# Kernel tuning notes

Hardware: AMD Instinct MI355X
Metric: run time of the kernel (lower is better)

Reference implementation:

```python
import jax, jax.numpy as jnp
import numpy as np

SAMPLE_RATE = 22050
N_FILTER_BANKS = 64
HOP_LENGTH = 512
BATCH = 4
N_FRAMES = 500
N_SAMPLES = N_FRAMES * HOP_LENGTH


def _frame_mean_weights(n_frames, n_samples):
    """Per-frame weights w s.t. mean over time of linear(align_corners=True)
    upsampling of a length-n_frames signal equals w @ signal (exact same math,
    since the interpolation is linear in the frame values)."""
    pos = jnp.linspace(0.0, n_frames - 1.0, n_samples)
    lo = jnp.clip(jnp.floor(pos).astype(jnp.int32), 0, n_frames - 2)
    frac = pos - lo
    w = jnp.zeros(n_frames, dtype=jnp.float32)
    w = w.at[lo].add(1.0 - frac).at[lo + 1].add(frac)
    return w / n_samples


def setup_inputs() -> dict:
    key = jax.random.key(0)
    k1, k2 = jax.random.split(key)
    filter_magnitudes = jax.random.uniform(k1, (BATCH, N_FRAMES, N_FILTER_BANKS), dtype=jnp.float32)
    noise = jax.random.normal(k2, (BATCH, N_SAMPLES), dtype=jnp.float32)
    return {"filter_magnitudes": filter_magnitudes, "noise": noise}


def reference(filter_magnitudes, noise):
    B, n_frames, n_banks = filter_magnitudes.shape
    n_samples = noise.shape[1]

    noise_fft = jnp.fft.rfft(noise, axis=1)                      # (B, n_freq) complex
    freqs = jnp.fft.rfftfreq(n_samples, 1.0 / SAMPLE_RATE)       # (n_freq,)
    filter_freqs = jnp.logspace(np.log10(20.0), np.log10(SAMPLE_RATE / 2.0), n_banks).astype(jnp.float32)

    # mean over time of the linearly-upsampled magnitudes (exact, no big buffer)
    mean_w = _frame_mean_weights(n_frames, n_samples)            # (n_frames,)
    mean_mag = jnp.einsum('bfk,f->bk', filter_magnitudes, mean_w)  # (B, n_banks)

    # vectorized log-distance filterbank weights: (n_freq, n_banks)
    D = jnp.log(freqs + 1e-7)[:, None] - jnp.log(filter_freqs + 1e-7)[None, :]
    W = jnp.exp(-(D ** 2) / 0.5)
    W = W / (W.sum(axis=1, keepdims=True) + 1e-7)

    filter_response = mean_mag @ W.T                              # (B, n_freq)
    filtered_fft = noise_fft * filter_response
    return jnp.fft.irfft(filtered_fft, n=n_samples, axis=1)      # (B, n_samples)
```

## Files before the change

kernel.cpp:

```cpp
#include <hip/hip_runtime.h>
#include <math.h>

#define NS 256000
#define N1 512
#define N2 500
#define PI_F 3.14159265358979323846f

typedef float2 cplx;

__device__ __forceinline__ cplx cadd(cplx a, cplx b){ return make_float2(a.x+b.x, a.y+b.y); }
__device__ __forceinline__ cplx csub(cplx a, cplx b){ return make_float2(a.x-b.x, a.y-b.y); }
__device__ __forceinline__ cplx cmul(cplx a, cplx b){ return make_float2(a.x*b.x-a.y*b.y, a.x*b.y+a.y*b.x); }
__device__ __forceinline__ cplx cmulc(cplx a, cplx b){ return make_float2(a.x*b.x+a.y*b.y, a.y*b.x-a.x*b.y); }
__device__ __forceinline__ cplx crotf(cplx v, float ang){
    float sn = __sinf(ang), cs = __cosf(ang);
    return make_float2(v.x*cs - v.y*sn, v.x*sn + v.y*cs);
}
__device__ __forceinline__ int PX(int e){ return e + (e>>4); }
__device__ __forceinline__ int rev8_3(int k){ return ((k&7)<<6) | (k&0x38) | (k>>6); }

#define U1PAD 545
#define U2PAD 537
#define WFENCE() asm volatile("s_waitcnt lgkmcnt(0)" ::: "memory")
#define LDS_BARRIER() do{ asm volatile("s_waitcnt lgkmcnt(0)" ::: "memory"); __builtin_amdgcn_s_barrier(); }while(0)

template<bool INV>
__device__ __forceinline__ void dft4(const cplx* a, cplx* b){
    cplx t0=cadd(a[0],a[2]), t1=csub(a[0],a[2]), t2=cadd(a[1],a[3]), t3=csub(a[1],a[3]);
    b[0]=cadd(t0,t2); b[2]=csub(t0,t2);
    if(!INV){ b[1]=make_float2(t1.x+t3.y, t1.y-t3.x); b[3]=make_float2(t1.x-t3.y, t1.y+t3.x); }
    else    { b[1]=make_float2(t1.x-t3.y, t1.y+t3.x); b[3]=make_float2(t1.x+t3.y, t1.y-t3.x); }
}

template<bool INV>
__device__ __forceinline__ void dft8(const cplx* a, cplx* b){
    cplx ev[4]={a[0],a[2],a[4],a[6]}, od[4]={a[1],a[3],a[5],a[7]};
    cplx C[4], D[4];
    dft4<INV>(ev, C); dft4<INV>(od, D);
    const float s = 0.70710678118654752f;
    const float sg = INV ? 1.f : -1.f;
    cplx d1 = cmul(D[1], make_float2( s, sg*s));
    cplx d2 = cmul(D[2], make_float2(0.f, sg ));
    cplx d3 = cmul(D[3], make_float2(-s, sg*s));
    b[0]=cadd(C[0],D[0]); b[4]=csub(C[0],D[0]);
    b[1]=cadd(C[1],d1);   b[5]=csub(C[1],d1);
    b[2]=cadd(C[2],d2);   b[6]=csub(C[2],d2);
    b[3]=cadd(C[3],d3);   b[7]=csub(C[3],d3);
}

template<bool INV>
__device__ __forceinline__ void dft5(const cplx* a, cplx* b){
    const float c1=0.30901699437494742f, s1=0.95105651629515357f;
    const float c2=-0.80901699437494745f, s2=0.58778525229247312f;
    const float sg = INV ? 1.f : -1.f;
    cplx W[5];
    W[0]=make_float2(1.f,0.f);
    W[1]=make_float2(c1, sg*s1); W[2]=make_float2(c2, sg*s2);
    W[3]=make_float2(c2,-sg*s2); W[4]=make_float2(c1,-sg*s1);
#pragma unroll
    for(int u=0;u<5;++u){
        cplx acc = a[0];
        int idx = 0;
#pragma unroll
        for(int r=1;r<5;++r){
            idx += u; if(idx >= 5) idx -= 5;
            acc = cadd(acc, cmul(a[r], W[idx]));
        }
        b[u] = acc;
    }
}

template<int R, int L, int TMUL, bool INV, int NN>
__device__ __forceinline__ void wstage(cplx* Uw, const cplx* tab, int lane){
    constexpr int m = L / R;
    constexpr int nb = NN / R;
    constexpr int NIT = (nb + 63) / 64;
    cplx a[NIT][R];
    cplx wt[NIT][R];
    int  bs[NIT];
#pragma unroll
    for(int it=0; it<NIT; ++it){
        int beta = lane + it*64;
        int blk = beta / m;
        int j = beta - blk*m;
        bs[it] = blk*L + j;
        if(beta < nb){
#pragma unroll
            for(int t=0;t<R;++t) a[it][t] = Uw[PX(bs[it] + m*t)];
#pragma unroll
            for(int t=1;t<R;++t) wt[it][t] = tab[TMUL*j*t];
        }
    }
#pragma unroll
    for(int it=0; it<NIT; ++it){
        int beta = lane + it*64;
        if(beta < nb){
            if(INV){
#pragma unroll
                for(int t=1;t<R;++t) a[it][t] = cmulc(a[it][t], wt[it][t]);
            }
            cplx bb[R];
            if constexpr (R==4) dft4<INV>(a[it], bb);
            else if constexpr (R==5) dft5<INV>(a[it], bb);
            else dft8<INV>(a[it], bb);
            if(!INV){
#pragma unroll
                for(int t=1;t<R;++t) bb[t] = cmul(bb[t], wt[it][t]);
            }
#pragma unroll
            for(int t=0;t<R;++t) Uw[PX(bs[it] + m*t)] = bb[t];
        }
    }
}

template<int R, int L, int TMUL, bool INV>
__device__ __forceinline__ void wstage2(cplx* Uc, const cplx* tab, int lane, int h){
    constexpr int m = L / R;
    constexpr int nb = 500 / R;
    constexpr int HB = (nb + 1) / 2;
    const int lim = h ? (nb - HB) : HB;
    if(lane < lim){
        int beta = h*HB + lane;
        int blk = beta / m;
        int j = beta - blk*m;
        int base = blk*L + j;
        cplx a[R];
#pragma unroll
        for(int t=0;t<R;++t) a[t] = Uc[PX(base + m*t)];
        cplx wt[R];
#pragma unroll
        for(int t=1;t<R;++t) wt[t] = tab[TMUL*j*t];
        if(INV){
#pragma unroll
            for(int t=1;t<R;++t) a[t] = cmulc(a[t], wt[t]);
        }
        cplx bb[R];
        if constexpr (R==4) dft4<INV>(a,bb);
        else if constexpr (R==5) dft5<INV>(a,bb);
        else dft8<INV>(a,bb);
        if(!INV){
#pragma unroll
            for(int t=1;t<R;++t) bb[t] = cmul(bb[t], wt[t]);
        }
#pragma unroll
        for(int t=0;t<R;++t) Uc[PX(base + m*t)] = bb[t];
    }
}

template<int NTAB, int NTHR>
__device__ __forceinline__ void build_tab(cplx* tab, int tid){
    const float step = -2.f*PI_F/(float)NTAB;
    for(int i = tid; i < NTAB; i += NTHR){
        float a = step*(float)i;
        tab[i] = make_float2(__cosf(a), __sinf(a));
    }
}

__device__ __forceinline__ int p2k2(int p){
    int t1 = p/100; int r = p - 100*t1;
    int t2 = r/20;  r -= 20*t2;
    int t3 = r>>2;  int t4 = r & 3;
    return t1 + 5*t2 + 25*t3 + 125*t4;
}
__device__ __forceinline__ int k22p(int k){
    int t1 = k % 5; int k5 = k/5;
    int t2 = k5 % 5; int k25 = k5/5;
    int t3 = k25 % 5; int t4 = k25/5;
    return 100*t1 + 20*t2 + 4*t3 + t4;
}
__device__ __forceinline__ int colord(int q){
    int j = q>>1, w = q&1;
    if(j == 0) return w ? 256 : 0;
    return w ? 512 - j : j;
}
__device__ __forceinline__ int xcd_chunk(int bid, int n){
    int q = n>>3, r = n&7;
    int x = bid&7, idx = bid>>3;
    return (x < r ? x*(q+1) : r*(q+1) + (x-r)*q) + idx;
}

__device__ __forceinline__ void hpair(cplx Z1, cplx Z2, float ha, float hb,
                                      cplx* zk, cplx* znk){
    float xr = 0.5f*(Z1.x + Z2.x), xi = 0.5f*(Z1.y - Z2.y);
    float yr = 0.5f*(Z1.y + Z2.y), yi = -0.5f*(Z1.x - Z2.x);
    *zk  = make_float2(ha*xr - hb*yi, ha*xi + hb*yr);
    *znk = make_float2(ha*xr + hb*yi, hb*yr - ha*xi);
}

__global__ void __launch_bounds__(256) kFused1(const float* __restrict__ fm,
                                               const float* __restrict__ noise,
                                               float* __restrict__ mmL,
                                               cplx* __restrict__ Y){
    __shared__ float Aarr[500];
    __shared__ float wfr[500];
    __shared__ float part[256];
    __shared__ cplx tab[512];
    __shared__ cplx U[4][U1PAD];
    const int bid = blockIdx.x, tid = threadIdx.x;
    if(bid < 4){
        const int b = bid;
        for(int f = tid; f < 500; f += 256){
            long long i0 = ((long long)f*255999LL + 498LL)/499LL;
            long long i1 = ((long long)(f+1)*255999LL + 498LL)/499LL;
            long long cnt = i1 - i0;
            long long sumi = (i0 + i1 - 1)*cnt/2;
            long long num = 499LL*sumi - cnt*(long long)f*255999LL;
            Aarr[f] = (float)((double)num / 255999.0);
        }
        __syncthreads();
        for(int f = tid; f < 500; f += 256){
            long long i0 = ((long long)f*255999LL + 498LL)/499LL;
            long long i1 = ((long long)(f+1)*255999LL + 498LL)/499LL;
            double w;
            if(f < 499) w = (double)(i1 - i0) - (double)Aarr[f] + (f > 0 ? (double)Aarr[f-1] : 0.0);
            else        w = (double)Aarr[498] + 1.0;
            wfr[f] = (float)(w / (double)NS);
        }
        __syncthreads();
        const int k = tid & 63, seg = tid >> 6;
        float acc = 0.f;
        for(int f = seg*125; f < seg*125 + 125; ++f)
            acc += wfr[f] * fm[(b*500 + f)*64 + k];
        part[seg*64 + k] = acc;
        __syncthreads();
        if(tid < 64) mmL[b*64 + tid] = part[tid] + part[64+tid] + part[128+tid] + part[192+tid];
        return;
    }
    if(bid == 4){
        if(tid < 64){
            double a = log10(20.0), b2 = log10(11025.0);
            double e = a + (b2 - a)*(double)tid/63.0;
            float ff = (float)pow(10.0, e);
            mmL[256 + tid] = logf(ff + 1e-7f);
        }
        return;
    }
    const int g = xcd_chunk(bid - 5, 250);
    const int s = g / 125;
    const int n2base = (g - s*125) * 4;
    const int lane = tid & 63, w = tid >> 6;
    build_tab<512,256>(tab, tid);
    const float* xa = noise + (size_t)(2*s)*NS + n2base;
    const float* xb = noise + (size_t)(2*s+1)*NS + n2base;
#pragma unroll
    for(int k=0;k<8;++k){
        int i = tid + 256*k;
        int n1 = i >> 2, ws = i & 3;
        U[ws][PX(n1)] = make_float2(xa[n1*500 + ws], xb[n1*500 + ws]);
    }
    __syncthreads();
    cplx* Uw = U[w];
    wstage<8,512, 1,false,512>(Uw, tab, lane); WFENCE();
    wstage<8, 64, 8,false,512>(Uw, tab, lane); WFENCE();
    wstage<8,  8,64,false,512>(Uw, tab, lane); WFENCE();
    const int n2 = n2base + w;
    cplx* yp = Y + ((size_t)s*500 + n2)*512;
    const float tw = -2.f*PI_F/(float)NS;
#pragma unroll
    for(int t=0;t<8;++t){
        int q = lane + 64*t;
        int c = colord(q);
        cplx v = Uw[PX(rev8_3(c))];
        v = crotf(v, tw*(float)(n2*c));
        yp[q] = v;
    }
}

__global__ void __launch_bounds__(256) kFused2(cplx* __restrict__ Y,
                                               const float* __restrict__ mmL){
    __shared__ cplx tab[500];
    __shared__ cplx U[2][U2PAD];
    __shared__ float Hr[4][500];
    __shared__ float mmS[2][64];
    __shared__ float lgf[64];
    const int tid = threadIdx.x, lane = tid & 63, W = tid >> 6;
    const int L = xcd_chunk(blockIdx.x, 512);
    const int s = L >> 8, blk = L & 255;
    cplx* yb = Y + (size_t)s*500*512 + 2*blk;
    cplx rg[4];
#pragma unroll
    for(int k=0;k<4;++k){
        int i = tid + 256*k;
        rg[k] = (i < 1000) ? yb[(i>>1)*512 + (i&1)] : make_float2(0.f, 0.f);
    }
    build_tab<500,256>(tab, tid);
    if(tid < 128) mmS[tid>>6][tid&63] = mmL[2*s*64 + tid];
    if(tid < 64)  lgf[tid] = mmL[256 + tid];
    LDS_BARRIER();
    const int nrows = (blk == 0) ? 2 : 1;
    const float invN = 1.f/(float)NS;
    for(int idx = tid; idx < nrows*500; idx += 256){
        int r = (idx >= 500) ? 1 : 0;
        int p = idx - 500*r;
        int k1 = (blk == 0) ? (r ? 256 : 0) : blk;
        int k2 = p2k2(p);
        int kf = k1 + 512*k2;
        int kk = min(kf, NS - kf);
        float lf = logf((float)kk*(22050.f/(float)NS) + 1e-7f);
        float wsum = 0.f, a0 = 0.f, a1 = 0.f;
#pragma unroll
        for(int jb=0;jb<64;++jb){
            float d = lf - lgf[jb];
            float e = __expf(-2.f*d*d);
            wsum += e; a0 += e*mmS[0][jb]; a1 += e*mmS[1][jb];
        }
        float inv = invN/(wsum + 1e-7f);
        Hr[0][p] = (r==0) ? a0*inv : Hr[0][p];
        if(r==0){ Hr[0][p] = a0*inv; Hr[1][p] = a1*inv; }
        else    { Hr[2][p] = a0*inv; Hr[3][p] = a1*inv; }
    }
#pragma unroll
    for(int k=0;k<4;++k){
        int i = tid + 256*k;
        if(i < 1000) U[i&1][PX(i>>1)] = rg[k];
    }
    __syncthreads();
    const int c = W >> 1, h = W & 1;
    cplx* Uc = U[c];
    wstage2<5,500,  1,false>(Uc, tab, lane, h); __syncthreads();
    wstage2<5,100,  5,false>(Uc, tab, lane, h); __syncthreads();
    wstage2<5, 20, 25,false>(Uc, tab, lane, h); __syncthreads();
    wstage2<4,  4,125,false>(Uc, tab, lane, h); __syncthreads();
    if(blk == 0){
        if(c == 0){
#pragma unroll
            for(int t=0;t<4;++t){
                int p = h*250 + lane + 64*t;
                if(lane + 64*t < 250){
                    int k2 = p2k2(p);
                    int pp = k22p((500 - k2) % 500);
                    if(p <= pp){
                        cplx Z1 = U[0][PX(p)], Z2 = U[0][PX(pp)];
                        cplx zk, znk;
                        hpair(Z1, Z2, Hr[0][p], Hr[1][p], &zk, &znk);
                        U[0][PX(p)]  = zk;
                        U[0][PX(pp)] = znk;
                    }
                }
            }
        } else {
#pragma unroll
            for(int t=0;t<2;++t){
                int pl = lane + 64*t;
                if(pl < 125){
                    int p = h*125 + pl;
                    cplx Z1 = U[1][PX(p)], Z2 = U[1][PX(499-p)];
                    cplx zk, znk;
                    hpair(Z1, Z2, Hr[2][p], Hr[3][p], &zk, &znk);
                    U[1][PX(p)]     = zk;
                    U[1][PX(499-p)] = znk;
                }
            }
        }
    } else {
#pragma unroll
        for(int t=0;t<2;++t){
            int pl = lane + 64*t;
            if(pl < 125){
                int p = W*125 + pl;
                cplx Z1 = U[0][PX(p)], Z2 = U[1][PX(499-p)];
                cplx zk, znk;
                hpair(Z1, Z2, Hr[0][p], Hr[1][p], &zk, &znk);
                U[0][PX(p)]     = zk;
                U[1][PX(499-p)] = znk;
            }
        }
    }
    __syncthreads();
    wstage2<4,  4,125,true>(Uc, tab, lane, h); __syncthreads();
    wstage2<5, 20, 25,true>(Uc, tab, lane, h); __syncthreads();
    wstage2<5,100,  5,true>(Uc, tab, lane, h); __syncthreads();
    wstage2<5,500,  1,true>(Uc, tab, lane, h); __syncthreads();
    const float tw = 2.f*PI_F/(float)NS;
#pragma unroll
    for(int k=0;k<4;++k){
        int i = tid + 256*k;
        if(i < 1000){
            int n2 = i >> 1, ws = i & 1;
            int cc = colord(2*blk + ws);
            cplx v = U[ws][PX(n2)];
            v = crotf(v, tw*(float)(n2*cc));
            yb[n2*512 + ws] = v;
        }
    }
}

__global__ void __launch_bounds__(256) kFused3(const cplx* __restrict__ Y,
                                               float* __restrict__ out){
    __shared__ cplx tab[512];
    __shared__ cplx U[4][U1PAD];
    const int tid = threadIdx.x, lane = tid & 63, w = tid >> 6;
    const int g = xcd_chunk(blockIdx.x, 250);
    const int s = g / 125;
    const int n2base = (g - s*125) * 4;
    build_tab<512,256>(tab, tid);
    const cplx* yp = Y + ((size_t)s*500 + n2base)*512;
#pragma unroll
    for(int k=0;k<8;++k){
        int i = tid + 256*k;
        int ws = i >> 9, q = i & 511;
        cplx v = yp[(size_t)ws*512 + q];
        U[ws][PX(rev8_3(colord(q)))] = v;
    }
    __syncthreads();
    cplx* Uw = U[w];
    wstage<8,  8,64,true,512>(Uw, tab, lane); WFENCE();
    wstage<8, 64, 8,true,512>(Uw, tab, lane); WFENCE();
    wstage<8,512, 1,true,512>(Uw, tab, lane); WFENCE();
    __syncthreads();
    float* oa = out + (size_t)(2*s)*NS + n2base;
    float* ob = out + (size_t)(2*s+1)*NS + n2base;
#pragma unroll
    for(int k=0;k<8;++k){
        int i = tid + 256*k;
        int n1 = i >> 2, ws = i & 3;
        cplx v = U[ws][PX(n1)];
        oa[n1*500 + ws] = v.x;
        ob[n1*500 + ws] = v.y;
    }
}

extern "C" void kernel_launch(void* const* d_in, const int* in_sizes, int n_in,
                              void* d_out, int out_size, void* d_ws, size_t ws_size,
                              hipStream_t stream) {
    const float* fm = (const float*)d_in[0];
    const float* noise = (const float*)d_in[1];
    float* out = (float*)d_out;

    char* ws = (char*)d_ws;
    cplx*  Y   = (cplx*)ws;
    float* mmL = (float*)(ws + 4200000);

    kFused1<<<255, 256, 0, stream>>>(fm, noise, mmL, Y);
    kFused2<<<512, 256, 0, stream>>>(Y, mmL);
    kFused3<<<250, 256, 0, stream>>>(Y, out);
}
```

Before: 93.45 us.

## Merge three FFT kernels into one cooperative kernel with grid syncs

Replaces the three separate FFT-stage launches with a single cooperative kernel of 256 blocks × 512 threads that uses grid.sync between the row FFT, the filtered column FFT, and the inverse row FFT. The intermediate Y buffer is transposed to a padded row length of 504 so each middle-stage block processes two column pairs, and the XCD chunk remapping is dropped. The aim is to remove launch gaps and inter-kernel drain. The cost is grid-wide barriers, half the threads idle during the 512-point stages, and more LDS per block, which may limit occupancy.

```diff
diff --git a/kernel.cpp b/kernel.cpp
--- a/kernel.cpp
+++ b/kernel.cpp
@@ -1,9 +1,13 @@
 #include <hip/hip_runtime.h>
+#include <hip/hip_cooperative_groups.h>
 #include <math.h>
+
+namespace cg = cooperative_groups;
 
 #define NS 256000
 #define N1 512
 #define N2 500
+#define YROW 504
 #define PI_F 3.14159265358979323846f
 
 typedef float2 cplx;
@@ -20,7 +24,6 @@
 __device__ __forceinline__ int rev8_3(int k){ return ((k&7)<<6) | (k&0x38) | (k>>6); }
 
 #define U1PAD 545
-#define U2PAD 537
 #define WFENCE() asm volatile("s_waitcnt lgkmcnt(0)" ::: "memory")
 #define LDS_BARRIER() do{ asm volatile("s_waitcnt lgkmcnt(0)" ::: "memory"); __builtin_amdgcn_s_barrier(); }while(0)
 
@@ -173,11 +176,6 @@
     if(j == 0) return w ? 256 : 0;
     return w ? 512 - j : j;
 }
-__device__ __forceinline__ int xcd_chunk(int bid, int n){
-    int q = n>>3, r = n&7;
-    int x = bid&7, idx = bid>>3;
-    return (x < r ? x*(q+1) : r*(q+1) + (x-r)*q) + idx;
-}
 
 __device__ __forceinline__ void hpair(cplx Z1, cplx Z2, float ha, float hb,
                                       cplx* zk, cplx* znk){
@@ -187,19 +185,56 @@
     *znk = make_float2(ha*xr + hb*yi, hb*yr - ha*xi);
 }
 
-__global__ void __launch_bounds__(256) kFused1(const float* __restrict__ fm,
-                                               const float* __restrict__ noise,
-                                               float* __restrict__ mmL,
-                                               cplx* __restrict__ Y){
+__global__ void __launch_bounds__(512) kMega(const float* __restrict__ fm,
+                                             const float* __restrict__ noise,
+                                             float* __restrict__ out,
+                                             cplx* __restrict__ Y,
+                                             float* __restrict__ mmL){
+    __shared__ cplx tab[512];
+    __shared__ cplx Ush[4*U1PAD];
+    __shared__ float HrS[2][4][500];
+    __shared__ float mmS[4][64];
+    __shared__ float lgf[64];
     __shared__ float Aarr[500];
     __shared__ float wfr[500];
     __shared__ float part[256];
-    __shared__ cplx tab[512];
-    __shared__ cplx U[4][U1PAD];
-    const int bid = blockIdx.x, tid = threadIdx.x;
-    if(bid < 4){
-        const int b = bid;
-        for(int f = tid; f < 500; f += 256){
+
+    cg::grid_group grid = cg::this_grid();
+    const int tid = threadIdx.x, lane = tid & 63, w = tid >> 6;
+    const int bid = blockIdx.x;
+
+    if(bid < 250){
+        const int s = bid/125, n2base = (bid - s*125)*4;
+        build_tab<512,512>(tab, tid);
+        const float* xa = noise + (size_t)(2*s)*NS + n2base;
+        const float* xb = noise + (size_t)(2*s+1)*NS + n2base;
+#pragma unroll
+        for(int k=0;k<4;++k){
+            int i = tid + 512*k;
+            int n1 = i >> 2, wc = i & 3;
+            Ush[wc*U1PAD + PX(n1)] = make_float2(xa[n1*500 + wc], xb[n1*500 + wc]);
+        }
+        __syncthreads();
+        if(w < 4){
+            cplx* Uw = Ush + w*U1PAD;
+            wstage<8,512, 1,false,512>(Uw, tab, lane); WFENCE();
+            wstage<8, 64, 8,false,512>(Uw, tab, lane); WFENCE();
+            wstage<8,  8,64,false,512>(Uw, tab, lane);
+        }
+        __syncthreads();
+        const float tw = -2.f*PI_F/(float)NS;
+#pragma unroll
+        for(int k=0;k<4;++k){
+            int i = tid + 512*k;
+            int q = i >> 2, wc = i & 3;
+            int cq = colord(q);
+            cplx v = Ush[wc*U1PAD + PX(rev8_3(cq))];
+            v = crotf(v, tw*(float)((n2base + wc)*cq));
+            Y[((size_t)s*512 + q)*YROW + n2base + wc] = v;
+        }
+    } else if(bid < 254){
+        const int b = bid - 250;
+        for(int f = tid; f < 500; f += 512){
             long long i0 = ((long long)f*255999LL + 498LL)/499LL;
             long long i1 = ((long long)(f+1)*255999LL + 498LL)/499LL;
             long long cnt = i1 - i0;
@@ -208,215 +243,189 @@
             Aarr[f] = (float)((double)num / 255999.0);
         }
         __syncthreads();
-        for(int f = tid; f < 500; f += 256){
+        for(int f = tid; f < 500; f += 512){
             long long i0 = ((long long)f*255999LL + 498LL)/499LL;
             long long i1 = ((long long)(f+1)*255999LL + 498LL)/499LL;
-            double w;
-            if(f < 499) w = (double)(i1 - i0) - (double)Aarr[f] + (f > 0 ? (double)Aarr[f-1] : 0.0);
-            else        w = (double)Aarr[498] + 1.0;
-            wfr[f] = (float)(w / (double)NS);
-        }
-        __syncthreads();
-        const int k = tid & 63, seg = tid >> 6;
-        float acc = 0.f;
-        for(int f = seg*125; f < seg*125 + 125; ++f)
-            acc += wfr[f] * fm[(b*500 + f)*64 + k];
-        part[seg*64 + k] = acc;
+            double ww;
+            if(f < 499) ww = (double)(i1 - i0) - (double)Aarr[f] + (f > 0 ? (double)Aarr[f-1] : 0.0);
+            else        ww = (double)Aarr[498] + 1.0;
+            wfr[f] = (float)(ww / (double)NS);
+        }
+        __syncthreads();
+        if(tid < 256){
+            const int k = tid & 63, seg = tid >> 6;
+            float acc = 0.f;
+            for(int f = seg*125; f < seg*125 + 125; ++f)
+                acc += wfr[f] * fm[(b*500 + f)*64 + k];
+            part[tid] = acc;
+        }
         __syncthreads();
         if(tid < 64) mmL[b*64 + tid] = part[tid] + part[64+tid] + part[128+tid] + part[192+tid];
-        return;
-    }
-    if(bid == 4){
+    } else if(bid == 254){
         if(tid < 64){
             double a = log10(20.0), b2 = log10(11025.0);
             double e = a + (b2 - a)*(double)tid/63.0;
             float ff = (float)pow(10.0, e);
             mmL[256 + tid] = logf(ff + 1e-7f);
         }
-        return;
-    }
-    const int g = xcd_chunk(bid - 5, 250);
-    const int s = g / 125;
-    const int n2base = (g - s*125) * 4;
-    const int lane = tid & 63, w = tid >> 6;
-    build_tab<512,256>(tab, tid);
-    const float* xa = noise + (size_t)(2*s)*NS + n2base;
-    const float* xb = noise + (size_t)(2*s+1)*NS + n2base;
-#pragma unroll
-    for(int k=0;k<8;++k){
-        int i = tid + 256*k;
-        int n1 = i >> 2, ws = i & 3;
-        U[ws][PX(n1)] = make_float2(xa[n1*500 + ws], xb[n1*500 + ws]);
-    }
-    __syncthreads();
-    cplx* Uw = U[w];
-    wstage<8,512, 1,false,512>(Uw, tab, lane); WFENCE();
-    wstage<8, 64, 8,false,512>(Uw, tab, lane); WFENCE();
-    wstage<8,  8,64,false,512>(Uw, tab, lane); WFENCE();
-    const int n2 = n2base + w;
-    cplx* yp = Y + ((size_t)s*500 + n2)*512;
-    const float tw = -2.f*PI_F/(float)NS;
-#pragma unroll
-    for(int t=0;t<8;++t){
-        int q = lane + 64*t;
-        int c = colord(q);
-        cplx v = Uw[PX(rev8_3(c))];
-        v = crotf(v, tw*(float)(n2*c));
-        yp[q] = v;
-    }
-}
-
-__global__ void __launch_bounds__(256) kFused2(cplx* __restrict__ Y,
-                                               const float* __restrict__ mmL){
-    __shared__ cplx tab[500];
-    __shared__ cplx U[2][U2PAD];
-    __shared__ float Hr[4][500];
-    __shared__ float mmS[2][64];
-    __shared__ float lgf[64];
-    const int tid = threadIdx.x, lane = tid & 63, W = tid >> 6;
-    const int L = xcd_chunk(blockIdx.x, 512);
-    const int s = L >> 8, blk = L & 255;
-    cplx* yb = Y + (size_t)s*500*512 + 2*blk;
-    cplx rg[4];
-#pragma unroll
-    for(int k=0;k<4;++k){
-        int i = tid + 256*k;
-        rg[k] = (i < 1000) ? yb[(i>>1)*512 + (i&1)] : make_float2(0.f, 0.f);
-    }
-    build_tab<500,256>(tab, tid);
-    if(tid < 128) mmS[tid>>6][tid&63] = mmL[2*s*64 + tid];
-    if(tid < 64)  lgf[tid] = mmL[256 + tid];
-    LDS_BARRIER();
-    const int nrows = (blk == 0) ? 2 : 1;
-    const float invN = 1.f/(float)NS;
-    for(int idx = tid; idx < nrows*500; idx += 256){
-        int r = (idx >= 500) ? 1 : 0;
-        int p = idx - 500*r;
-        int k1 = (blk == 0) ? (r ? 256 : 0) : blk;
-        int k2 = p2k2(p);
-        int kf = k1 + 512*k2;
-        int kk = min(kf, NS - kf);
-        float lf = logf((float)kk*(22050.f/(float)NS) + 1e-7f);
-        float wsum = 0.f, a0 = 0.f, a1 = 0.f;
-#pragma unroll
-        for(int jb=0;jb<64;++jb){
-            float d = lf - lgf[jb];
-            float e = __expf(-2.f*d*d);
-            wsum += e; a0 += e*mmS[0][jb]; a1 += e*mmS[1][jb];
-        }
-        float inv = invN/(wsum + 1e-7f);
-        Hr[0][p] = (r==0) ? a0*inv : Hr[0][p];
-        if(r==0){ Hr[0][p] = a0*inv; Hr[1][p] = a1*inv; }
-        else    { Hr[2][p] = a0*inv; Hr[3][p] = a1*inv; }
-    }
-#pragma unroll
-    for(int k=0;k<4;++k){
-        int i = tid + 256*k;
-        if(i < 1000) U[i&1][PX(i>>1)] = rg[k];
-    }
-    __syncthreads();
-    const int c = W >> 1, h = W & 1;
-    cplx* Uc = U[c];
-    wstage2<5,500,  1,false>(Uc, tab, lane, h); __syncthreads();
-    wstage2<5,100,  5,false>(Uc, tab, lane, h); __syncthreads();
-    wstage2<5, 20, 25,false>(Uc, tab, lane, h); __syncthreads();
-    wstage2<4,  4,125,false>(Uc, tab, lane, h); __syncthreads();
-    if(blk == 0){
-        if(c == 0){
-#pragma unroll
-            for(int t=0;t<4;++t){
-                int p = h*250 + lane + 64*t;
-                if(lane + 64*t < 250){
-                    int k2 = p2k2(p);
-                    int pp = k22p((500 - k2) % 500);
-                    if(p <= pp){
-                        cplx Z1 = U[0][PX(p)], Z2 = U[0][PX(pp)];
-                        cplx zk, znk;
-                        hpair(Z1, Z2, Hr[0][p], Hr[1][p], &zk, &znk);
-                        U[0][PX(p)]  = zk;
-                        U[0][PX(pp)] = znk;
+    }
+    __threadfence();
+    grid.sync();
+
+    {
+        const int utid = tid & 255;
+        const int pu = tid >> 8;
+        const int uw = (tid >> 6) & 3;
+        const int c  = uw >> 1, h = uw & 1;
+        const int gp = 2*bid + pu;
+        const int su = gp >> 8, blk = gp & 255;
+        cplx* yb0 = Y + ((size_t)su*512 + 2*blk)*YROW;
+        cplx rg[4];
+#pragma unroll
+        for(int k=0;k<4;++k){
+            int e = utid + 256*k;
+            int row = (e >= 500) ? 1 : 0;
+            int n2 = e - 500*row;
+            rg[k] = (e < 1000) ? yb0[(size_t)row*YROW + n2] : make_float2(0.f,0.f);
+        }
+        build_tab<500,512>(tab, tid);
+        if(tid < 256) ((float*)mmS)[tid] = mmL[tid];
+        if(tid < 64)  lgf[tid] = mmL[256 + tid];
+        LDS_BARRIER();
+        const int nrows = (blk == 0) ? 2 : 1;
+        const float invN = 1.f/(float)NS;
+        for(int idx = utid; idx < nrows*500; idx += 256){
+            int r = (idx >= 500) ? 1 : 0;
+            int p = idx - 500*r;
+            int k1 = (blk == 0) ? (r ? 256 : 0) : blk;
+            int k2 = p2k2(p);
+            int kf = k1 + 512*k2;
+            int kk = min(kf, NS - kf);
+            float lf = logf((float)kk*(22050.f/(float)NS) + 1e-7f);
+            float wsum = 0.f, a0 = 0.f, a1 = 0.f;
+#pragma unroll
+            for(int jb=0;jb<64;++jb){
+                float d = lf - lgf[jb];
+                float e2 = __expf(-2.f*d*d);
+                wsum += e2; a0 += e2*mmS[2*su][jb]; a1 += e2*mmS[2*su+1][jb];
+            }
+            float inv = invN/(wsum + 1e-7f);
+            if(r==0){ HrS[pu][0][p] = a0*inv; HrS[pu][1][p] = a1*inv; }
+            else    { HrS[pu][2][p] = a0*inv; HrS[pu][3][p] = a1*inv; }
+        }
+#pragma unroll
+        for(int k=0;k<4;++k){
+            int e = utid + 256*k;
+            if(e < 1000){
+                int row = (e >= 500) ? 1 : 0;
+                int n2 = e - 500*row;
+                Ush[(pu*2 + row)*U1PAD + PX(n2)] = rg[k];
+            }
+        }
+        __syncthreads();
+        cplx* Uc = Ush + (pu*2 + c)*U1PAD;
+        wstage2<5,500,  1,false>(Uc, tab, lane, h); __syncthreads();
+        wstage2<5,100,  5,false>(Uc, tab, lane, h); __syncthreads();
+        wstage2<5, 20, 25,false>(Uc, tab, lane, h); __syncthreads();
+        wstage2<4,  4,125,false>(Uc, tab, lane, h); __syncthreads();
+        cplx* UA = Ush + (pu*2 + 0)*U1PAD;
+        cplx* UB = Ush + (pu*2 + 1)*U1PAD;
+        float (*Hp)[500] = HrS[pu];
+        if(blk == 0){
+            if(c == 0){
+#pragma unroll 1
+                for(int t=0;t<4;++t){
+                    int pl = lane + 64*t;
+                    if(pl < 250){
+                        int p = h*250 + pl;
+                        int k2 = p2k2(p);
+                        int pp = k22p((500 - k2) % 500);
+                        if(p <= pp){
+                            cplx Z1 = UA[PX(p)], Z2 = UA[PX(pp)];
+                            cplx zk, znk;
+                            hpair(Z1, Z2, Hp[0][p], Hp[1][p], &zk, &znk);
+                            UA[PX(p)]  = zk;
+                            UA[PX(pp)] = znk;
+                        }
                     }
                 }
+            } else {
+#pragma unroll 1
+                for(int t=0;t<2;++t){
+                    int pl = lane + 64*t;
+                    if(pl < 125){
+                        int p = h*125 + pl;
+                        cplx Z1 = UB[PX(p)], Z2 = UB[PX(499-p)];
+                        cplx zk, znk;
+                        hpair(Z1, Z2, Hp[2][p], Hp[3][p], &zk, &znk);
+                        UB[PX(p)]     = zk;
+                        UB[PX(499-p)] = znk;
+                    }
+                }
             }
         } else {
-#pragma unroll
+#pragma unroll 1
             for(int t=0;t<2;++t){
                 int pl = lane + 64*t;
                 if(pl < 125){
-                    int p = h*125 + pl;
-                    cplx Z1 = U[1][PX(p)], Z2 = U[1][PX(499-p)];
+                    int p = uw*125 + pl;
+                    cplx Z1 = UA[PX(p)], Z2 = UB[PX(499-p)];
                     cplx zk, znk;
-                    hpair(Z1, Z2, Hr[2][p], Hr[3][p], &zk, &znk);
-                    U[1][PX(p)]     = zk;
-                    U[1][PX(499-p)] = znk;
+                    hpair(Z1, Z2, Hp[0][p], Hp[1][p], &zk, &znk);
+                    UA[PX(p)]     = zk;
+                    UB[PX(499-p)] = znk;
                 }
             }
         }
-    } else {
-#pragma unroll
-        for(int t=0;t<2;++t){
-            int pl = lane + 64*t;
-            if(pl < 125){
-                int p = W*125 + pl;
-                cplx Z1 = U[0][PX(p)], Z2 = U[1][PX(499-p)];
-                cplx zk, znk;
-                hpair(Z1, Z2, Hr[0][p], Hr[1][p], &zk, &znk);
-                U[0][PX(p)]     = zk;
-                U[1][PX(499-p)] = znk;
-            }
-        }
-    }
-    __syncthreads();
-    wstage2<4,  4,125,true>(Uc, tab, lane, h); __syncthreads();
-    wstage2<5, 20, 25,true>(Uc, tab, lane, h); __syncthreads();
-    wstage2<5,100,  5,true>(Uc, tab, lane, h); __syncthreads();
-    wstage2<5,500,  1,true>(Uc, tab, lane, h); __syncthreads();
-    const float tw = 2.f*PI_F/(float)NS;
-#pragma unroll
-    for(int k=0;k<4;++k){
-        int i = tid + 256*k;
-        if(i < 1000){
-            int n2 = i >> 1, ws = i & 1;
-            int cc = colord(2*blk + ws);
-            cplx v = U[ws][PX(n2)];
-            v = crotf(v, tw*(float)(n2*cc));
-            yb[n2*512 + ws] = v;
-        }
-    }
-}
-
-__global__ void __launch_bounds__(256) kFused3(const cplx* __restrict__ Y,
-                                               float* __restrict__ out){
-    __shared__ cplx tab[512];
-    __shared__ cplx U[4][U1PAD];
-    const int tid = threadIdx.x, lane = tid & 63, w = tid >> 6;
-    const int g = xcd_chunk(blockIdx.x, 250);
-    const int s = g / 125;
-    const int n2base = (g - s*125) * 4;
-    build_tab<512,256>(tab, tid);
-    const cplx* yp = Y + ((size_t)s*500 + n2base)*512;
-#pragma unroll
-    for(int k=0;k<8;++k){
-        int i = tid + 256*k;
-        int ws = i >> 9, q = i & 511;
-        cplx v = yp[(size_t)ws*512 + q];
-        U[ws][PX(rev8_3(colord(q)))] = v;
-    }
-    __syncthreads();
-    cplx* Uw = U[w];
-    wstage<8,  8,64,true,512>(Uw, tab, lane); WFENCE();
-    wstage<8, 64, 8,true,512>(Uw, tab, lane); WFENCE();
-    wstage<8,512, 1,true,512>(Uw, tab, lane); WFENCE();
-    __syncthreads();
-    float* oa = out + (size_t)(2*s)*NS + n2base;
-    float* ob = out + (size_t)(2*s+1)*NS + n2base;
-#pragma unroll
-    for(int k=0;k<8;++k){
-        int i = tid + 256*k;
-        int n1 = i >> 2, ws = i & 3;
-        cplx v = U[ws][PX(n1)];
-        oa[n1*500 + ws] = v.x;
-        ob[n1*500 + ws] = v.y;
+        __syncthreads();
+        wstage2<4,  4,125,true>(Uc, tab, lane, h); __syncthreads();
+        wstage2<5, 20, 25,true>(Uc, tab, lane, h); __syncthreads();
+        wstage2<5,100,  5,true>(Uc, tab, lane, h); __syncthreads();
+        wstage2<5,500,  1,true>(Uc, tab, lane, h); __syncthreads();
+        const float tw2 = 2.f*PI_F/(float)NS;
+#pragma unroll
+        for(int k=0;k<4;++k){
+            int e = utid + 256*k;
+            if(e < 1000){
+                int row = (e >= 500) ? 1 : 0;
+                int n2 = e - 500*row;
+                int cc = colord(2*blk + row);
+                cplx v = Ush[(pu*2 + row)*U1PAD + PX(n2)];
+                v = crotf(v, tw2*(float)(n2*cc));
+                yb0[(size_t)row*YROW + n2] = v;
+            }
+        }
+    }
+    __threadfence();
+    grid.sync();
+
+    if(bid < 250){
+        const int s = bid/125, n2base = (bid - s*125)*4;
+        build_tab<512,512>(tab, tid);
+#pragma unroll
+        for(int k=0;k<4;++k){
+            int i = tid + 512*k;
+            int q = i >> 2, wc = i & 3;
+            Ush[wc*U1PAD + PX(rev8_3(colord(q)))] = Y[((size_t)s*512 + q)*YROW + n2base + wc];
+        }
+        __syncthreads();
+        if(w < 4){
+            cplx* Uw = Ush + w*U1PAD;
+            wstage<8,  8,64,true,512>(Uw, tab, lane); WFENCE();
+            wstage<8, 64, 8,true,512>(Uw, tab, lane); WFENCE();
+            wstage<8,512, 1,true,512>(Uw, tab, lane);
+        }
+        __syncthreads();
+        float* oa = out + (size_t)(2*s)*NS + n2base;
+        float* ob = out + (size_t)(2*s+1)*NS + n2base;
+#pragma unroll
+        for(int k=0;k<4;++k){
+            int i = tid + 512*k;
+            int n1 = i >> 2, wc = i & 3;
+            cplx v = Ush[wc*U1PAD + PX(n1)];
+            oa[n1*500 + wc] = v.x;
+            ob[n1*500 + wc] = v.y;
+        }
     }
 }
 
@@ -427,11 +436,10 @@
     const float* noise = (const float*)d_in[1];
     float* out = (float*)d_out;
 
-    char* ws = (char*)d_ws;
-    cplx*  Y   = (cplx*)ws;
-    float* mmL = (float*)(ws + 4200000);
-
-    kFused1<<<255, 256, 0, stream>>>(fm, noise, mmL, Y);
-    kFused2<<<512, 256, 0, stream>>>(Y, mmL);
-    kFused3<<<250, 256, 0, stream>>>(Y, out);
-}
+    char* wsb = (char*)d_ws;
+    cplx*  Y   = (cplx*)wsb;
+    float* mmL = (float*)(wsb + 4194304);
+
+    void* args[] = { (void*)&fm, (void*)&noise, (void*)&out, (void*)&Y, (void*)&mmL };
+    hipLaunchCooperativeKernel((void*)kMega, dim3(256), dim3(512), args, 0, stream);
+}
```

Result: slower. 260.8 us (+179.1%).
